# Kernel tuning notes

Measured on AMD Instinct MI355X. Metric: run time of the kernel, lower is better.

## Reference

```python
import jax, jax.numpy as jnp
import numpy as np

N, NFEAT, NHID, NCLASS, NIDX = 200000, 512, 128, 70, 10000


def normalize_l2(X):
    # row L2-normalize; norm is detached in the original (stop_gradient),
    # inf scale (zero rows) mapped to 0
    rownorm = jax.lax.stop_gradient(jnp.linalg.norm(X, axis=1, keepdims=True))
    scale = jnp.where(rownorm > 0, 1.0 / rownorm, 0.0)
    return X * scale


def setup_inputs() -> dict:
    key = jax.random.key(0)
    ks = jax.random.split(key, 9)
    x = jax.random.normal(ks[0], (N, NFEAT), dtype=jnp.float32)
    simple_features = jax.random.normal(ks[1], (N, NFEAT), dtype=jnp.float32)
    idx = jax.random.randint(ks[2], (NIDX,), 0, N)
    s = 0.05
    W0 = jax.random.normal(ks[3], (NHID, NFEAT), dtype=jnp.float32) * s
    W1 = jax.random.normal(ks[4], (NHID, NFEAT), dtype=jnp.float32) * s
    G1 = jax.random.normal(ks[5], (NHID, NHID), dtype=jnp.float32) * s
    G2 = jax.random.normal(ks[6], (NHID, NHID), dtype=jnp.float32) * s
    GT = jax.random.normal(ks[7], (NHID, 2 * NHID), dtype=jnp.float32) * s
    Wc = jax.random.normal(ks[8], (NCLASS, NHID), dtype=jnp.float32) * s
    return {"x": x, "simple_features": simple_features, "idx": idx,
            "W0": W0, "W1": W1, "G1": G1, "G2": G2, "GT": GT, "Wc": Wc}


def reference(x, simple_features, idx, W0, W1, G1, G2, GT, Wc):
    x = normalize_l2(x)                      # [N, nfeat]
    sf = normalize_l2(simple_features)       # [N, nfeat]
    # dropout/dropout_adj are identity (p=0)
    layer_inner = jax.nn.relu(x @ W0.T)      # [N, nhid]
    lay_simple = jax.nn.relu(sf @ W1.T)      # [N, nhid]
    gate1 = layer_inner @ G1.T               # [N, nhid]
    gate2 = lay_simple @ G2.T                # [N, nhid]
    gate = jax.nn.sigmoid(jnp.concatenate([gate1, gate2], axis=1) @ GT.T)
    fix_inner = (1.0 - gate) * layer_inner + gate * lay_simple
    fix_inner = normalize_l2(fix_inner)
    logits = jax.nn.relu(fix_inner @ Wc.T)   # [N, nclass]
    return jax.nn.log_softmax(logits, axis=-1)[idx]
```

## Files before the change

### kernel.cpp

```cpp
#include <hip/hip_runtime.h>
#include <math.h>

#define NFEAT  512
#define NHID   128
#define NCLASS 70
#define NIDX   10000
#define NTILE  625
#define NT2    313
#define HELEMS (2u * NIDX * NHID)
#define WIMG_ELEMS (2u * 128 * 512)
#define SMALL_ELEMS 74496u
#define WS_NEED ((size_t)(HELEMS + WIMG_ELEMS + SMALL_ELEMS) * 2)

typedef float  f32x4  __attribute__((ext_vector_type(4)));
typedef __bf16 bf16x8 __attribute__((ext_vector_type(8)));

static __device__ __forceinline__ unsigned short f2bf(float f) {
    unsigned u = __builtin_bit_cast(unsigned, f);
    u += 0x7fffu + ((u >> 16) & 1u);
    return (unsigned short)(u >> 16);
}
static __device__ __forceinline__ float bf2f(unsigned short h) {
    unsigned u = ((unsigned)h) << 16;
    return __builtin_bit_cast(float, u);
}
static __device__ __forceinline__ bf16x8 pack8(float4 a, float4 b) {
    bf16x8 r;
    r[0] = (__bf16)a.x; r[1] = (__bf16)a.y; r[2] = (__bf16)a.z; r[3] = (__bf16)a.w;
    r[4] = (__bf16)b.x; r[5] = (__bf16)b.y; r[6] = (__bf16)b.z; r[7] = (__bf16)b.w;
    return r;
}
static __device__ __forceinline__ bf16x8 pack8s(float4 a, float4 b, float s) {
    bf16x8 r;
    r[0] = (__bf16)(a.x * s); r[1] = (__bf16)(a.y * s); r[2] = (__bf16)(a.z * s); r[3] = (__bf16)(a.w * s);
    r[4] = (__bf16)(b.x * s); r[5] = (__bf16)(b.y * s); r[6] = (__bf16)(b.z * s); r[7] = (__bf16)(b.w * s);
    return r;
}
static __device__ __forceinline__ f32x4 MFMA(bf16x8 a, bf16x8 b, f32x4 c) {
    return __builtin_amdgcn_mfma_f32_16x16x32_bf16(a, b, c, 0, 0, 0);
}
static __device__ __forceinline__ bf16x8 ldsAx(const unsigned short* base, int row, int colb, int rstride) {
    return *(const bf16x8*)((const char*)base + row * rstride + (colb ^ ((row & 7) << 4)));
}
static __device__ __forceinline__ void ldsW1(unsigned short* base, int row, int col, unsigned short v) {
    *(unsigned short*)((char*)base + row * 256 + ((col * 2) ^ ((row & 7) << 4))) = v;
}
static __device__ __forceinline__ float ldsR1(const unsigned short* base, int row, int col) {
    return bf2f(*(const unsigned short*)((const char*)base + row * 256 + ((col * 2) ^ ((row & 7) << 4))));
}

__global__ void prep_weights(const float* __restrict__ W0, const float* __restrict__ W1,
                             const float* __restrict__ G1, const float* __restrict__ G2,
                             const float* __restrict__ GT, const float* __restrict__ Wc,
                             unsigned short* __restrict__ wsWimg,
                             unsigned short* __restrict__ wsSmall) {
    int i = blockIdx.x * 256 + threadIdx.x;
    if (i < 16384) {
        int t = i >> 13;
        int r = i & 8191;
        int n = r >> 6, k8 = r & 63;
        const float* src = (t ? W1 : W0) + (size_t)n * NFEAT + k8 * 8;
        float4 a = ((const float4*)src)[0], b = ((const float4*)src)[1];
        char* dst = (char*)wsWimg + t * 131072 + n * 1024 + ((k8 * 16) ^ ((n & 7) << 4));
        *(bf16x8*)dst = pack8(a, b);
    } else {
        int i4 = i - 16384;
        if (i4 >= 18624) return;
        const float* src; int base4, dstb;
        if      (i4 < 4096)  { src = G1; base4 = 0;     dstb = 0; }
        else if (i4 < 8192)  { src = G2; base4 = 4096;  dstb = 16384; }
        else if (i4 < 16384) { src = GT; base4 = 8192;  dstb = 32768; }
        else                 { src = Wc; base4 = 16384; dstb = 65536; }
        float4 v = ((const float4*)src)[i4 - base4];
        ushort4 o;
        o.x = f2bf(v.x); o.y = f2bf(v.y); o.z = f2bf(v.z); o.w = f2bf(v.w);
        *(ushort4*)(wsSmall + dstb + (size_t)(i4 - base4) * 4) = o;
    }
}

__global__ __launch_bounds__(512) void stageB_ws(
    const float* __restrict__ x, const float* __restrict__ sf,
    const int* __restrict__ idx,
    const unsigned short* __restrict__ wsWimg,
    unsigned short* __restrict__ wsH)
{
    __shared__ __align__(16) unsigned short Wl[65536];
    __shared__ __align__(16) unsigned short Xl[8192];
    __shared__ __align__(16) unsigned short Hl[2048];

    const int tid  = threadIdx.x;
    const int w    = tid >> 6;
    const int lane = tid & 63;
    const int ln   = lane & 15, lg = lane >> 4;
    const int bid  = blockIdx.x;
    const int t    = bid / 125, tb = bid % 125;
    const int tile0 = tb * 5;
    const float* XS = t ? sf : x;
    const f32x4 zero4 = {0.f, 0.f, 0.f, 0.f};

    float4 ga0, ga1, gb0, gb1;
    {
        int r0 = idx[tile0 * 16 + w];
        int r1 = idx[tile0 * 16 + w + 8];
        const float4* p0 = (const float4*)(XS + (size_t)r0 * NFEAT + lane * 8);
        const float4* p1 = (const float4*)(XS + (size_t)r1 * NFEAT + lane * 8);
        ga0 = p0[0]; ga1 = p0[1];
        gb0 = p1[0]; gb1 = p1[1];
    }
    {
        const uint4* src = (const uint4*)((const char*)wsWimg + (size_t)t * 131072);
        uint4* dst = (uint4*)Wl;
        #pragma unroll
        for (int i = 0; i < 16; ++i) dst[tid + i * 512] = src[tid + i * 512];
    }
    auto putX = [&](int m, float4 a, float4 b) {
        float ss = a.x*a.x + a.y*a.y + a.z*a.z + a.w*a.w
                 + b.x*b.x + b.y*b.y + b.z*b.z + b.w*b.w;
        #pragma unroll
        for (int d = 1; d < 64; d <<= 1) ss += __shfl_xor(ss, d);
        float scl = (ss > 0.f) ? (1.f / sqrtf(ss)) : 0.f;
        *(bf16x8*)((char*)Xl + m * 1024 + ((lane * 16) ^ ((m & 7) << 4))) = pack8s(a, b, scl);
    };
    putX(w,     ga0, ga1);
    putX(w + 8, gb0, gb1);
    __syncthreads();

    for (int it = 0; it < 5; ++it) {
        float4 na0, na1, nb0, nb1;
        if (it < 4) {
            int tile = tile0 + it + 1;
            int r0 = idx[tile * 16 + w];
            int r1 = idx[tile * 16 + w + 8];
            const float4* p0 = (const float4*)(XS + (size_t)r0 * NFEAT + lane * 8);
            const float4* p1 = (const float4*)(XS + (size_t)r1 * NFEAT + lane * 8);
            na0 = p0[0]; na1 = p0[1];
            nb0 = p1[0]; nb1 = p1[1];
        }
        f32x4 accE = zero4, accO = zero4;
        #pragma unroll
        for (int kc = 0; kc < 16; ++kc) {
            bf16x8 a = ldsAx(Xl, ln,          kc * 64 + lg * 16, 1024);
            bf16x8 b = ldsAx(Wl, w * 16 + ln, kc * 64 + lg * 16, 1024);
            if (kc & 1) accO = MFMA(a, b, accO); else accE = MFMA(a, b, accE);
        }
        f32x4 acc = accE + accO;
        #pragma unroll
        for (int rg = 0; rg < 4; ++rg)
            ldsW1(Hl, lg * 4 + rg, w * 16 + ln, f2bf(fmaxf(acc[rg], 0.f)));
        __syncthreads();

        if (tid < 256) {
            int tile = tile0 + it;
            ((uint4*)(wsH + ((size_t)t * NIDX + (size_t)tile * 16) * NHID))[tid]
                = ((const uint4*)Hl)[tid];
        }
        if (it < 4) {
            putX(w,     na0, na1);
            putX(w + 8, nb0, nb1);
        }
        __syncthreads();
    }
}

__global__ __launch_bounds__(512) void tailCDE2(
    const unsigned short* __restrict__ wsSmall,
    const unsigned short* __restrict__ wsH,
    float* __restrict__ out)
{
    __shared__ __align__(16) unsigned short Hbuf[2][2][16][NHID];
    __shared__ __align__(16) unsigned short G12s[2][2][16][NHID];
    __shared__ __align__(16) unsigned short FIXs[2][16][NHID];
    __shared__ float scl2[2][16];

    const unsigned short* G1p = wsSmall;
    const unsigned short* G2p = wsSmall + 16384;
    const unsigned short* GTp = wsSmall + 32768;
    const unsigned short* Wcp = wsSmall + 65536;

    const int tid  = threadIdx.x;
    const int bid  = blockIdx.x;
    const int w    = tid >> 6;
    const int lane = tid & 63;
    const int ln   = lane & 15, lg = lane >> 4;
    const int tB = w >> 2, nq = w & 3;
    const f32x4 zero4 = {0.f, 0.f, 0.f, 0.f};
    const int tile0 = bid * 2;
    const int tileC1 = (tile0 + 1 < NTILE) ? tile0 + 1 : NTILE - 1;

    {
        int tt = tid >> 8, r = tid & 255;
        uint4 v0 = *(const uint4*)((const char*)wsH
                + ((size_t)tt * NIDX + (size_t)tile0 * 16) * 256 + r * 16);
        uint4 v1 = *(const uint4*)((const char*)wsH
                + ((size_t)tt * NIDX + (size_t)tileC1 * 16) * 256 + r * 16);
        ((uint4*)&Hbuf[0][0][0][0])[tid] = v0;
        ((uint4*)&Hbuf[1][0][0][0])[tid] = v1;
    }
    bf16x8 cf[8];
    {
        const unsigned short* Gp = tB ? G2p : G1p;
        #pragma unroll
        for (int kc = 0; kc < 4; ++kc)
            #pragma unroll
            for (int nt = 0; nt < 2; ++nt)
                cf[kc * 2 + nt] = *(const bf16x8*)(Gp + (size_t)(nq * 32 + nt * 16 + ln) * NHID + kc * 32 + lg * 8);
    }
    const int nD = w * 16 + ln;
    bf16x8 gt[8];
    #pragma unroll
    for (int kc = 0; kc < 8; ++kc)
        gt[kc] = *(const bf16x8*)(GTp + (size_t)nD * (2 * NHID) + kc * 32 + lg * 8);
    __syncthreads();

    #pragma unroll
    for (int ti = 0; ti < 2; ++ti) {
        const unsigned short* Hs = &Hbuf[ti][tB][0][0];
        f32x4 accC[2] = {zero4, zero4};
        #pragma unroll
        for (int kc = 0; kc < 4; ++kc) {
            bf16x8 a = ldsAx(Hs, ln, kc * 64 + lg * 16, 256);
            accC[0] = MFMA(a, cf[kc * 2],     accC[0]);
            accC[1] = MFMA(a, cf[kc * 2 + 1], accC[1]);
        }
        unsigned short* Gd = &G12s[ti][tB][0][0];
        #pragma unroll
        for (int nt = 0; nt < 2; ++nt)
            #pragma unroll
            for (int rg = 0; rg < 4; ++rg) {
                int m = lg * 4 + rg;
                ldsW1(Gd, m, nq * 32 + nt * 16 + ln, f2bf(accC[nt][rg]));
            }
    }
    const int ccE = w * 16 + ln;
    const int ccl = (ccE < NCLASS) ? ccE : 0;
    bf16x8 wcf[4];
    #pragma unroll
    for (int kc = 0; kc < 4; ++kc)
        wcf[kc] = *(const bf16x8*)(Wcp + (size_t)ccl * NHID + kc * 32 + lg * 8);
    __syncthreads();

    #pragma unroll
    for (int ti = 0; ti < 2; ++ti) {
        f32x4 aE = zero4, aO = zero4;
        #pragma unroll
        for (int kc = 0; kc < 8; ++kc) {
            const unsigned short* As = &G12s[ti][kc >> 2][0][0];
            bf16x8 a = ldsAx(As, ln, (kc & 3) * 64 + lg * 16, 256);
            if (kc & 1) aO = MFMA(a, gt[kc], aO); else aE = MFMA(a, gt[kc], aE);
        }
        f32x4 accD = aE + aO;
        #pragma unroll
        for (int rg = 0; rg < 4; ++rg) {
            int m = lg * 4 + rg;
            float g  = 1.f / (1.f + __expf(-accD[rg]));
            float h0 = ldsR1(&Hbuf[ti][0][0][0], m, nD);
            float h1 = ldsR1(&Hbuf[ti][1][0][0], m, nD);
            ldsW1(&FIXs[ti][0][0], m, nD, f2bf((1.f - g) * h0 + g * h1));
        }
    }
    __syncthreads();

    {
        int rr = tid >> 4, sl = tid & 15;
        int ti = rr >> 4, r = rr & 15;
        bf16x8 v = ldsAx(&FIXs[ti][0][0], r, sl * 16, 256);
        float ss = 0.f;
        #pragma unroll
        for (int j = 0; j < 8; ++j) { float f = (float)v[j]; ss += f * f; }
        ss += __shfl_xor(ss, 1); ss += __shfl_xor(ss, 2);
        ss += __shfl_xor(ss, 4); ss += __shfl_xor(ss, 8);
        if (sl == 0) scl2[ti][r] = (ss > 0.f) ? (1.f / sqrtf(ss)) : 0.f;
    }
    __syncthreads();

    if (w < 5) {
        const bool live = (ccE < NCLASS);
        bf16x8 bfz;
        #pragma unroll
        for (int j = 0; j < 8; ++j) bfz[j] = (__bf16)0.f;
        #pragma unroll
        for (int ti = 0; ti < 2; ++ti) {
            f32x4 accE = zero4;
            #pragma unroll
            for (int kc = 0; kc < 4; ++kc) {
                bf16x8 a = ldsAx(&FIXs[ti][0][0], ln, kc * 64 + lg * 16, 256);
                accE = MFMA(a, live ? wcf[kc] : bfz, accE);
            }
            if (live) {
                float* LO = (float*)((char*)&G12s[0][0][0][0] + ti * 8192);
                #pragma unroll
                for (int rg = 0; rg < 4; ++rg) {
                    int m = lg * 4 + rg;
                    LO[m * 80 + ccE] = fmaxf(accE[rg] * scl2[ti][m], 0.f);
                }
            }
        }
    }
    __syncthreads();

    {
        int rr = tid >> 4, l16 = tid & 15;
        int ti = rr >> 4, r = rr & 15;
        const float* LO = (const float*)((const char*)&G12s[0][0][0][0] + ti * 8192) + r * 80;
        float v[5];
        #pragma unroll
        for (int j = 0; j < 5; ++j) {
            int c = l16 + j * 16;
            v[j] = (c < NCLASS) ? LO[c] : -1e30f;
        }
        float mx = v[0];
        #pragma unroll
        for (int j = 1; j < 5; ++j) mx = fmaxf(mx, v[j]);
        mx = fmaxf(mx, __shfl_xor(mx, 1)); mx = fmaxf(mx, __shfl_xor(mx, 2));
        mx = fmaxf(mx, __shfl_xor(mx, 4)); mx = fmaxf(mx, __shfl_xor(mx, 8));
        float se = 0.f;
        #pragma unroll
        for (int j = 0; j < 5; ++j) {
            int c = l16 + j * 16;
            if (c < NCLASS) se += __expf(v[j] - mx);
        }
        se += __shfl_xor(se, 1); se += __shfl_xor(se, 2);
        se += __shfl_xor(se, 4); se += __shfl_xor(se, 8);
        float lz = mx + __logf(se);
        int tile = tile0 + ti;
        if (tile < NTILE) {
            size_t orow = (size_t)tile * 16 + r;
            #pragma unroll
            for (int j = 0; j < 5; ++j) {
                int c = l16 + j * 16;
                if (c < NCLASS) out[orow * NCLASS + c] = v[j] - lz;
            }
        }
    }
}

static __device__ __forceinline__ bf16x8 bfragF(const float* p, size_t off) {
    const float4* q = (const float4*)(p + off);
    return pack8(q[0], q[1]);
}
__global__ __launch_bounds__(512) void hyper_fb(
    const float* __restrict__ x, const float* __restrict__ sf,
    const int* __restrict__ idx,
    const float* __restrict__ W0, const float* __restrict__ W1,
    const float* __restrict__ G1, const float* __restrict__ G2,
    const float* __restrict__ GT, const float* __restrict__ Wc,
    float* __restrict__ out)
{
    __shared__ __align__(16) unsigned short Xbuf[2][16][NFEAT];
    __shared__ __align__(16) unsigned short Hbuf[2][16][NHID];
    __shared__ float scl2[16];
    unsigned short* G12 = &Xbuf[0][0][0];
    unsigned short* FIX = &Xbuf[0][0][0] + 4096;
    float*          LOG = (float*)(&Xbuf[0][0][0] + 6144);

    const int tid = threadIdx.x, bid = blockIdx.x;
    const int w = tid >> 6, lane = tid & 63;
    const int ln = lane & 15, lg = lane >> 4;
    const int tB = w >> 2, nq = w & 3;
    const f32x4 zero4 = {0.f, 0.f, 0.f, 0.f};

    {
        char* xb = (char*)&Xbuf[0][0][0];
        #pragma unroll
        for (int j = 0; j < 4; ++j) {
            int p = w * 4 + j, t = p >> 4, m = p & 15;
            int ri = idx[bid * 16 + m];
            const float4* q = (const float4*)((t ? sf : x) + (size_t)ri * NFEAT + lane * 8);
            float4 a = q[0], b = q[1];
            float ss = a.x*a.x + a.y*a.y + a.z*a.z + a.w*a.w
                     + b.x*b.x + b.y*b.y + b.z*b.z + b.w*b.w;
            #pragma unroll
            for (int d = 1; d < 64; d <<= 1) ss += __shfl_xor(ss, d);
            float scl = (ss > 0.f) ? (1.f / sqrtf(ss)) : 0.f;
            int soff = t * 16384 + m * 1024 + ((lane * 16) ^ ((m & 7) << 4));
            *(bf16x8*)(xb + soff) = pack8s(a, b, scl);
        }
    }
    __syncthreads();
    {
        const float* Wp = tB ? W1 : W0;
        f32x4 acc0 = zero4, acc1 = zero4;
        const unsigned short* Xb = (const unsigned short*)((const char*)&Xbuf[0][0][0] + tB * 16384);
        #pragma unroll
        for (int kc = 0; kc < 16; ++kc) {
            bf16x8 a = ldsAx(Xb, ln, kc * 64 + lg * 16, 1024);
            acc0 = MFMA(a, bfragF(Wp, (size_t)(nq * 32 + ln) * NFEAT + kc * 32 + lg * 8), acc0);
            acc1 = MFMA(a, bfragF(Wp, (size_t)(nq * 32 + 16 + ln) * NFEAT + kc * 32 + lg * 8), acc1);
        }
        unsigned short* Hb = &Hbuf[tB][0][0];
        #pragma unroll
        for (int rg = 0; rg < 4; ++rg) {
            int m = lg * 4 + rg;
            ldsW1(Hb, m, nq * 32 + ln,      f2bf(fmaxf(acc0[rg], 0.f)));
            ldsW1(Hb, m, nq * 32 + 16 + ln, f2bf(fmaxf(acc1[rg], 0.f)));
        }
    }
    __syncthreads();
    {
        const float* Gp = tB ? G2 : G1;
        const unsigned short* Hs = &Hbuf[tB][0][0];
        f32x4 accC[2] = {zero4, zero4};
        #pragma unroll
        for (int kc = 0; kc < 4; ++kc) {
            bf16x8 a = ldsAx(Hs, ln, kc * 64 + lg * 16, 256);
            accC[0] = MFMA(a, bfragF(Gp, (size_t)(nq * 32 + ln) * NHID + kc * 32 + lg * 8), accC[0]);
            accC[1] = MFMA(a, bfragF(Gp, (size_t)(nq * 32 + 16 + ln) * NHID + kc * 32 + lg * 8), accC[1]);
        }
        unsigned short* Gd = G12 + tB * 2048;
        #pragma unroll
        for (int nt = 0; nt < 2; ++nt)
            #pragma unroll
            for (int rg = 0; rg < 4; ++rg) {
                int m = lg * 4 + rg;
                ldsW1(Gd, m, nq * 32 + nt * 16 + ln, f2bf(accC[nt][rg]));
            }
    }
    __syncthreads();
    {
        f32x4 accD = zero4;
        const int n = w * 16 + ln;
        #pragma unroll
        for (int kc = 0; kc < 8; ++kc) {
            const unsigned short* As = G12 + (kc >> 2) * 2048;
            bf16x8 a = ldsAx(As, ln, (kc & 3) * 64 + lg * 16, 256);
            accD = MFMA(a, bfragF(GT, (size_t)n * (2 * NHID) + kc * 32 + lg * 8), accD);
        }
        #pragma unroll
        for (int rg = 0; rg < 4; ++rg) {
            int m = lg * 4 + rg;
            float g  = 1.f / (1.f + __expf(-accD[rg]));
            float h0 = ldsR1(&Hbuf[0][0][0], m, n);
            float h1 = ldsR1(&Hbuf[1][0][0], m, n);
            ldsW1(FIX, m, n, f2bf((1.f - g) * h0 + g * h1));
        }
    }
    __syncthreads();
    if (tid < 256) {
        int r = tid >> 4, sl = tid & 15;
        bf16x8 v = ldsAx(FIX, r, sl * 16, 256);
        float ss = 0.f;
        #pragma unroll
        for (int j = 0; j < 8; ++j) { float f = (float)v[j]; ss += f * f; }
        ss += __shfl_xor(ss, 1); ss += __shfl_xor(ss, 2);
        ss += __shfl_xor(ss, 4); ss += __shfl_xor(ss, 8);
        if (sl == 0) scl2[r] = (ss > 0.f) ? (1.f / sqrtf(ss)) : 0.f;
    }
    __syncthreads();
    if (w < 5) {
        const int cc = w * 16 + ln;
        bf16x8 bfz;
        #pragma unroll
        for (int j = 0; j < 8; ++j) bfz[j] = (__bf16)0.f;
        f32x4 accE = zero4;
        #pragma unroll
        for (int kc = 0; kc < 4; ++kc) {
            bf16x8 a = ldsAx(FIX, ln, kc * 64 + lg * 16, 256);
            bf16x8 b = (cc < NCLASS) ? bfragF(Wc, (size_t)cc * NHID + kc * 32 + lg * 8) : bfz;
            accE = MFMA(a, b, accE);
        }
        #pragma unroll
        for (int rg = 0; rg < 4; ++rg) {
            int m = lg * 4 + rg;
            float v = fmaxf(accE[rg] * scl2[m], 0.f);
            LOG[m * 80 + cc] = (cc < NCLASS) ? v : -1e30f;
        }
    }
    __syncthreads();
    {
        const int r = tid >> 5, l32 = tid & 31;
        float v0 = LOG[r * 80 + l32];
        float v1 = LOG[r * 80 + 32 + l32];
        float v2 = (l32 < 16) ? LOG[r * 80 + 64 + l32] : -1e30f;
        float mx = fmaxf(fmaxf(v0, v1), v2);
        #pragma unroll
        for (int d = 1; d < 32; d <<= 1) mx = fmaxf(mx, __shfl_xor(mx, d, 32));
        float se = __expf(v0 - mx) + __expf(v1 - mx) + ((l32 < 16) ? __expf(v2 - mx) : 0.f);
        #pragma unroll
        for (int d = 1; d < 32; d <<= 1) se += __shfl_xor(se, d, 32);
        float lz = mx + __logf(se);
        size_t orow = (size_t)bid * 16 + r;
        out[orow * NCLASS + l32] = v0 - lz;
        if (l32 + 32 < NCLASS) out[orow * NCLASS + 32 + l32] = v1 - lz;
        if (l32 + 64 < NCLASS) out[orow * NCLASS + 64 + l32] = v2 - lz;
    }
}

extern "C" void kernel_launch(void* const* d_in, const int* in_sizes, int n_in,
                              void* d_out, int out_size, void* d_ws, size_t ws_size,
                              hipStream_t stream)
{
    const float* x   = (const float*)d_in[0];
    const float* sf  = (const float*)d_in[1];
    const int*   idx = (const int*)d_in[2];
    const float* W0  = (const float*)d_in[3];
    const float* W1  = (const float*)d_in[4];
    const float* G1  = (const float*)d_in[5];
    const float* G2  = (const float*)d_in[6];
    const float* GT  = (const float*)d_in[7];
    const float* Wc  = (const float*)d_in[8];
    float* out = (float*)d_out;

    if (ws_size >= WS_NEED) {
        unsigned short* wsH     = (unsigned short*)d_ws;
        unsigned short* wsWimg  = wsH + HELEMS;
        unsigned short* wsSmall = wsWimg + WIMG_ELEMS;
        prep_weights<<<dim3(137), dim3(256), 0, stream>>>(W0, W1, G1, G2, GT, Wc, wsWimg, wsSmall);
        stageB_ws<<<dim3(250), dim3(512), 0, stream>>>(x, sf, idx, wsWimg, wsH);
        tailCDE2<<<dim3(NT2), dim3(512), 0, stream>>>(wsSmall, wsH, out);
    } else {
        hyper_fb<<<dim3(NTILE), dim3(512), 0, stream>>>(
            x, sf, idx, W0, W1, G1, G2, GT, Wc, out);
    }
}
```

Measured before the change: 37.17 us.

## Move gate projection G1/G2 matmul into stage B and pass gates via workspace

Computes the gate1/gate2 projections (H @ G1^T, H @ G2^T) inside the first-layer kernel right after each H tile is produced, while it is still in LDS. The results go to a new workspace buffer. The tail kernel then loads both H and the precomputed G tiles instead of running the C-stage matmul, which removes one sync and the G-weight loads there. In exchange, stage B does extra MFMA work and LDS traffic per tile, and the workspace reads and writes grow by another 2·NIDX·NHID bf16 array.

```diff
diff --git a/kernel.cpp b/kernel.cpp
--- a/kernel.cpp
+++ b/kernel.cpp
@@ -8,9 +8,10 @@
 #define NTILE  625
 #define NT2    313
 #define HELEMS (2u * NIDX * NHID)
+#define GELEMS (2u * NIDX * NHID)
 #define WIMG_ELEMS (2u * 128 * 512)
 #define SMALL_ELEMS 74496u
-#define WS_NEED ((size_t)(HELEMS + WIMG_ELEMS + SMALL_ELEMS) * 2)
+#define WS_NEED ((size_t)(HELEMS + GELEMS + WIMG_ELEMS + SMALL_ELEMS) * 2)
 
 typedef float  f32x4  __attribute__((ext_vector_type(4)));
 typedef __bf16 bf16x8 __attribute__((ext_vector_type(8)));
@@ -78,15 +79,18 @@
     }
 }
 
-__global__ __launch_bounds__(512) void stageB_ws(
+__global__ __launch_bounds__(512) void stageBC(
     const float* __restrict__ x, const float* __restrict__ sf,
     const int* __restrict__ idx,
     const unsigned short* __restrict__ wsWimg,
-    unsigned short* __restrict__ wsH)
+    const unsigned short* __restrict__ wsSmall,
+    unsigned short* __restrict__ wsH,
+    unsigned short* __restrict__ wsG)
 {
     __shared__ __align__(16) unsigned short Wl[65536];
     __shared__ __align__(16) unsigned short Xl[8192];
     __shared__ __align__(16) unsigned short Hl[2048];
+    __shared__ __align__(16) unsigned short Gl[2048];
 
     const int tid  = threadIdx.x;
     const int w    = tid >> 6;
@@ -106,6 +110,13 @@
         const float4* p1 = (const float4*)(XS + (size_t)r1 * NFEAT + lane * 8);
         ga0 = p0[0]; ga1 = p0[1];
         gb0 = p1[0]; gb1 = p1[1];
+    }
+    bf16x8 cf[4];
+    {
+        const unsigned short* Gsm = wsSmall + t * 16384;
+        #pragma unroll
+        for (int kc = 0; kc < 4; ++kc)
+            cf[kc] = *(const bf16x8*)(Gsm + (size_t)(w * 16 + ln) * NHID + kc * 32 + lg * 8);
     }
     {
         const uint4* src = (const uint4*)((const char*)wsWimg + (size_t)t * 131072);
@@ -149,6 +160,12 @@
             ldsW1(Hl, lg * 4 + rg, w * 16 + ln, f2bf(fmaxf(acc[rg], 0.f)));
         __syncthreads();
 
+        f32x4 aC = zero4;
+        #pragma unroll
+        for (int kc = 0; kc < 4; ++kc) {
+            bf16x8 a = ldsAx(Hl, ln, kc * 64 + lg * 16, 256);
+            aC = MFMA(a, cf[kc], aC);
+        }
         if (tid < 256) {
             int tile = tile0 + it;
             ((uint4*)(wsH + ((size_t)t * NIDX + (size_t)tile * 16) * NHID))[tid]
@@ -158,13 +175,23 @@
             putX(w,     na0, na1);
             putX(w + 8, nb0, nb1);
         }
+        #pragma unroll
+        for (int rg = 0; rg < 4; ++rg)
+            ldsW1(Gl, lg * 4 + rg, w * 16 + ln, f2bf(aC[rg]));
         __syncthreads();
-    }
-}
-
-__global__ __launch_bounds__(512) void tailCDE2(
+
+        if (tid < 256) {
+            int tile = tile0 + it;
+            ((uint4*)(wsG + ((size_t)t * NIDX + (size_t)tile * 16) * NHID))[tid]
+                = ((const uint4*)Gl)[tid];
+        }
+    }
+}
+
+__global__ __launch_bounds__(512) void tailDE2(
     const unsigned short* __restrict__ wsSmall,
     const unsigned short* __restrict__ wsH,
+    const unsigned short* __restrict__ wsG,
     float* __restrict__ out)
 {
     __shared__ __align__(16) unsigned short Hbuf[2][2][16][NHID];
@@ -172,8 +199,6 @@
     __shared__ __align__(16) unsigned short FIXs[2][16][NHID];
     __shared__ float scl2[2][16];
 
-    const unsigned short* G1p = wsSmall;
-    const unsigned short* G2p = wsSmall + 16384;
     const unsigned short* GTp = wsSmall + 32768;
     const unsigned short* Wcp = wsSmall + 65536;
 
@@ -182,55 +207,24 @@
     const int w    = tid >> 6;
     const int lane = tid & 63;
     const int ln   = lane & 15, lg = lane >> 4;
-    const int tB = w >> 2, nq = w & 3;
     const f32x4 zero4 = {0.f, 0.f, 0.f, 0.f};
     const int tile0 = bid * 2;
-    const int tileC1 = (tile0 + 1 < NTILE) ? tile0 + 1 : NTILE - 1;
-
-    {
-        int tt = tid >> 8, r = tid & 255;
-        uint4 v0 = *(const uint4*)((const char*)wsH
-                + ((size_t)tt * NIDX + (size_t)tile0 * 16) * 256 + r * 16);
-        uint4 v1 = *(const uint4*)((const char*)wsH
-                + ((size_t)tt * NIDX + (size_t)tileC1 * 16) * 256 + r * 16);
-        ((uint4*)&Hbuf[0][0][0][0])[tid] = v0;
-        ((uint4*)&Hbuf[1][0][0][0])[tid] = v1;
-    }
-    bf16x8 cf[8];
-    {
-        const unsigned short* Gp = tB ? G2p : G1p;
-        #pragma unroll
-        for (int kc = 0; kc < 4; ++kc)
-            #pragma unroll
-            for (int nt = 0; nt < 2; ++nt)
-                cf[kc * 2 + nt] = *(const bf16x8*)(Gp + (size_t)(nq * 32 + nt * 16 + ln) * NHID + kc * 32 + lg * 8);
+    const int tiles[2] = { tile0, (tile0 + 1 < NTILE) ? tile0 + 1 : NTILE - 1 };
+
+    #pragma unroll
+    for (int i = 0; i < 2; ++i) {
+        int q = tid + i * 512;
+        int seg = q >> 8, r = q & 255;
+        int ti = seg >> 1, tt = seg & 1;
+        size_t off = ((size_t)tt * NIDX + (size_t)tiles[ti] * 16) * NHID;
+        ((uint4*)&Hbuf[0][0][0][0])[q] = ((const uint4*)(wsH + off))[r];
+        ((uint4*)&G12s[0][0][0][0])[q] = ((const uint4*)(wsG + off))[r];
     }
     const int nD = w * 16 + ln;
     bf16x8 gt[8];
     #pragma unroll
     for (int kc = 0; kc < 8; ++kc)
         gt[kc] = *(const bf16x8*)(GTp + (size_t)nD * (2 * NHID) + kc * 32 + lg * 8);
-    __syncthreads();
-
-    #pragma unroll
-    for (int ti = 0; ti < 2; ++ti) {
-        const unsigned short* Hs = &Hbuf[ti][tB][0][0];
-        f32x4 accC[2] = {zero4, zero4};
-        #pragma unroll
-        for (int kc = 0; kc < 4; ++kc) {
-            bf16x8 a = ldsAx(Hs, ln, kc * 64 + lg * 16, 256);
-            accC[0] = MFMA(a, cf[kc * 2],     accC[0]);
-            accC[1] = MFMA(a, cf[kc * 2 + 1], accC[1]);
-        }
-        unsigned short* Gd = &G12s[ti][tB][0][0];
-        #pragma unroll
-        for (int nt = 0; nt < 2; ++nt)
-            #pragma unroll
-            for (int rg = 0; rg < 4; ++rg) {
-                int m = lg * 4 + rg;
-                ldsW1(Gd, m, nq * 32 + nt * 16 + ln, f2bf(accC[nt][rg]));
-            }
-    }
     const int ccE = w * 16 + ln;
     const int ccl = (ccE < NCLASS) ? ccE : 0;
     bf16x8 wcf[4];
@@ -502,11 +496,12 @@
 
     if (ws_size >= WS_NEED) {
         unsigned short* wsH     = (unsigned short*)d_ws;
-        unsigned short* wsWimg  = wsH + HELEMS;
+        unsigned short* wsG     = wsH + HELEMS;
+        unsigned short* wsWimg  = wsG + GELEMS;
         unsigned short* wsSmall = wsWimg + WIMG_ELEMS;
         prep_weights<<<dim3(137), dim3(256), 0, stream>>>(W0, W1, G1, G2, GT, Wc, wsWimg, wsSmall);
-        stageB_ws<<<dim3(250), dim3(512), 0, stream>>>(x, sf, idx, wsWimg, wsH);
-        tailCDE2<<<dim3(NT2), dim3(512), 0, stream>>>(wsSmall, wsH, out);
+        stageBC<<<dim3(250), dim3(512), 0, stream>>>(x, sf, idx, wsWimg, wsSmall, wsH, wsG);
+        tailDE2<<<dim3(NT2), dim3(512), 0, stream>>>(wsSmall, wsH, wsG, out);
     } else {
         hyper_fb<<<dim3(NTILE), dim3(512), 0, stream>>>(
             x, sf, idx, W0, W1, G1, G2, GT, Wc, out);
```

Result: no change. 36.95 us (-0.6%).
